# Performance work log

Measured on AMD Instinct MI355X. Metric: run time of the kernel, lower is better.

Reference implementation:

```python
import jax, jax.numpy as jnp
import numpy as np

CHUNK = 2048  # query points processed per step; bounds peak memory at [CHUNK, F, 3]


def _safe_div(num, den):
    den_s = jnp.where(jnp.abs(den) > 1e-12, den, 1.0)
    return num / den_s


def _closest_point_on_triangle(p, a, b, c):
    """Ericson's region-based closest point on triangle.
    p: [n,1,3], a/b/c: [1,F,3] -> returns [n,F,3]."""
    ab = b - a
    ac = c - a
    ap = p - a
    d1 = jnp.sum(ab * ap, -1)
    d2 = jnp.sum(ac * ap, -1)
    bp = p - b
    d3 = jnp.sum(ab * bp, -1)
    d4 = jnp.sum(ac * bp, -1)
    cpv = p - c
    d5 = jnp.sum(ab * cpv, -1)
    d6 = jnp.sum(ac * cpv, -1)
    vc = d1 * d4 - d3 * d2
    vb = d5 * d2 - d1 * d6
    va = d3 * d6 - d5 * d4
    v_ab = jnp.clip(_safe_div(d1, d1 - d3), 0.0, 1.0)
    w_ac = jnp.clip(_safe_div(d2, d2 - d6), 0.0, 1.0)
    w_bc = jnp.clip(_safe_div(d4 - d3, (d4 - d3) + (d5 - d6)), 0.0, 1.0)
    denom = va + vb + vc
    v = _safe_div(vb, denom)
    w = _safe_div(vc, denom)
    res = a + ab * v[..., None] + ac * w[..., None]  # face interior
    m_bc = (va <= 0) & ((d4 - d3) >= 0) & ((d5 - d6) >= 0)
    m_ac = (vb <= 0) & (d2 >= 0) & (d6 <= 0)
    m_ab = (vc <= 0) & (d1 >= 0) & (d3 <= 0)
    m_c = (d6 >= 0) & (d5 <= d6)
    m_b = (d3 >= 0) & (d4 <= d3)
    m_a = (d1 <= 0) & (d2 <= 0)
    res = jnp.where(m_bc[..., None], b + w_bc[..., None] * (c - b), res)
    res = jnp.where(m_ac[..., None], a + w_ac[..., None] * ac, res)
    res = jnp.where(m_ab[..., None], a + v_ab[..., None] * ab, res)
    res = jnp.where(m_c[..., None], c, res)
    res = jnp.where(m_b[..., None], b, res)
    res = jnp.where(m_a[..., None], a, res)
    return res


def _query_one_batch(tris, pts):
    # tris: [F,3,3], pts: [Q,3]
    a, b, c = tris[:, 0], tris[:, 1], tris[:, 2]

    def chunk_fn(pc):  # pc: [CHUNK,3]
        cp = _closest_point_on_triangle(pc[:, None, :], a[None], b[None], c[None])  # [CHUNK,F,3]
        d2 = jnp.sum((pc[:, None, :] - cp) ** 2, -1)  # [CHUNK,F] squared distances
        dist = jnp.min(d2, axis=-1)
        idx = jnp.argmin(d2, axis=-1)
        closest = jnp.take_along_axis(cp, idx[:, None, None], axis=1)[:, 0]
        return dist, closest, idx.astype(jnp.int32)

    Q = pts.shape[0]
    pts_c = pts.reshape(Q // CHUNK, CHUNK, 3)
    dist, closest, idx = jax.lax.map(chunk_fn, pts_c)
    return dist.reshape(Q), closest.reshape(Q, 3), idx.reshape(Q)


def setup_inputs() -> dict:
    key = jax.random.key(0)
    k1, k2 = jax.random.split(key)
    triangles = jax.random.normal(k1, (2, 4096, 3, 3), dtype=jnp.float32)
    points = jax.random.normal(k2, (2, 16384, 3), dtype=jnp.float32)
    return {"triangles": triangles, "points": points}


def reference(triangles, points):
    # distances are SQUARED point-to-mesh distances, matching the CUDA kernel
    distances, closest_points, closest_faces = jax.vmap(_query_one_batch)(triangles, points)
    return distances, closest_points, closest_faces
```

## Files before the change

### kernel.cpp

```cpp
#include <hip/hip_runtime.h>
#include <math.h>

namespace {

typedef float v2f __attribute__((ext_vector_type(2)));

constexpr int B = 2;
constexpr int F = 4096;
constexpr int Q = 16384;
constexpr int NP = B * Q;
constexpr int BLOCK = 256;
constexpr int P = 2;

constexpr int OFF_DIST = 0;
constexpr int OFF_CP = NP;
constexpr int OFF_FACE = 4 * NP;


__device__ __forceinline__ float safediv(float num, float den) {
  #pragma clang fp contract(off)
  float d = (fabsf(den) > 1e-12f) ? den : 1.0f;
  return num / d;
}

__device__ __forceinline__ float clamp01(float x) {
  return fminf(fmaxf(x, 0.0f), 1.0f);
}

__device__ __forceinline__ void closest_pt(
    float px, float py, float pz,
    float ax, float ay, float az,
    float bx, float by, float bz,
    float cx, float cy, float cz,
    float& rx, float& ry, float& rz) {
  #pragma clang fp contract(off)
  float abx = bx - ax, aby = by - ay, abz = bz - az;
  float acx = cx - ax, acy = cy - ay, acz = cz - az;
  float apx = px - ax, apy = py - ay, apz = pz - az;
  float d1 = (abx * apx + aby * apy) + abz * apz;
  float d2 = (acx * apx + acy * apy) + acz * apz;
  float bpx = px - bx, bpy = py - by, bpz = pz - bz;
  float d3 = (abx * bpx + aby * bpy) + abz * bpz;
  float d4 = (acx * bpx + acy * bpy) + acz * bpz;
  float cpx = px - cx, cpy = py - cy, cpz = pz - cz;
  float d5 = (abx * cpx + aby * cpy) + abz * cpz;
  float d6 = (acx * cpx + acy * cpy) + acz * cpz;

  float vc = d1 * d4 - d3 * d2;
  float vb = d5 * d2 - d1 * d6;
  float va = d3 * d6 - d5 * d4;

  float v_ab = clamp01(safediv(d1, d1 - d3));
  float w_ac = clamp01(safediv(d2, d2 - d6));
  float w_bc = clamp01(safediv(d4 - d3, (d4 - d3) + (d5 - d6)));

  float denom = (va + vb) + vc;
  float v = safediv(vb, denom);
  float w = safediv(vc, denom);

  float ox = ax + abx * v + acx * w;
  float oy = ay + aby * v + acy * w;
  float oz = az + abz * v + acz * w;

  bool m_bc = (va <= 0.0f) && (d4 - d3 >= 0.0f) && (d5 - d6 >= 0.0f);
  bool m_ac = (vb <= 0.0f) && (d2 >= 0.0f) && (d6 <= 0.0f);
  bool m_ab = (vc <= 0.0f) && (d1 >= 0.0f) && (d3 <= 0.0f);
  bool m_c  = (d6 >= 0.0f) && (d5 <= d6);
  bool m_b  = (d3 >= 0.0f) && (d4 <= d3);
  bool m_a  = (d1 <= 0.0f) && (d2 <= 0.0f);

  if (m_bc) { ox = bx + w_bc * (cx - bx); oy = by + w_bc * (cy - by); oz = bz + w_bc * (cz - bz); }
  if (m_ac) { ox = ax + w_ac * acx;       oy = ay + w_ac * acy;       oz = az + w_ac * acz; }
  if (m_ab) { ox = ax + v_ab * abx;       oy = ay + v_ab * aby;       oz = az + v_ab * abz; }
  if (m_c)  { ox = cx; oy = cy; oz = cz; }
  if (m_b)  { ox = bx; oy = by; oz = bz; }
  if (m_a)  { ox = ax; oy = ay; oz = az; }

  rx = ox; ry = oy; rz = oz;
}

__device__ __forceinline__ float exact_d2(
    float px, float py, float pz, const float* __restrict__ g ) {
  #pragma clang fp contract(off)
  float rx, ry, rz;
  closest_pt(px, py, pz,
             g[0], g[1], g[2], g[3], g[4], g[5], g[6], g[7], g[8],
             rx, ry, rz);
  float dx = px - rx, dy = py - ry, dz = pz - rz;
  return (dx * dx + dy * dy) + dz * dz;
}


__device__ __forceinline__ void ins4(unsigned key,
    unsigned& K1, unsigned& K2, unsigned& K3, unsigned& K4) {
  bool b1 = key < K1, b2 = key < K2, b3 = key < K3, b4 = key < K4;
  K4 = b3 ? K3 : (b4 ? key : K4);
  K3 = b2 ? K2 : (b3 ? key : K3);
  K2 = b1 ? K1 : (b2 ? key : K2);
  K1 = b1 ? key : K1;
}

__device__ __forceinline__ void ins8(unsigned key,
    unsigned& K1, unsigned& K2, unsigned& K3, unsigned& K4,
    unsigned& K5, unsigned& K6, unsigned& K7, unsigned& K8) {
  bool b1 = key < K1, b2 = key < K2, b3 = key < K3, b4 = key < K4;
  bool b5 = key < K5, b6 = key < K6, b7 = key < K7, b8 = key < K8;
  K8 = b7 ? K7 : (b8 ? key : K8);
  K7 = b6 ? K6 : (b7 ? key : K7);
  K6 = b5 ? K5 : (b6 ? key : K6);
  K5 = b4 ? K4 : (b5 ? key : K5);
  K4 = b3 ? K3 : (b4 ? key : K4);
  K3 = b2 ? K2 : (b3 ? key : K3);
  K2 = b1 ? K1 : (b2 ? key : K2);
  K1 = b1 ? key : K1;
}


__device__ __forceinline__ unsigned screen_fin(
    float dint, float tabm, float tacm, float tbcm,
    float td1, float td2, float ap2m, float bp2, float t43d,
    float va, float vb, float vc,
    float aa, float bb, float cc, float pp, int idx) {
  float tab = __builtin_amdgcn_fmed3f(tabm, 0.0f, 1.0f);
  float sab = fmaf(-tab, fmaf(-tab, aa, td1), ap2m);
  float tac = __builtin_amdgcn_fmed3f(tacm, 0.0f, 1.0f);
  float sac = fmaf(-tac, fmaf(-tac, bb, td2), ap2m);
  float tbc = __builtin_amdgcn_fmed3f(tbcm, 0.0f, 1.0f);
  float sbc = fmaf(-tbc, fmaf(-tbc, cc, t43d), bp2);
  float dseg = fminf(fminf(sab, sac), sbc);
  float mv   = fminf(fminf(va, vb), vc);
  float d = (mv > 0.0f) ? dint : dseg;
  d = fmaxf(d + pp, 0.0f);
  return (__float_as_uint(d) & 0xFFFFF000u) | (unsigned)idx;
}

template <int NC>
__global__ __launch_bounds__(BLOCK, 4) void bvh_screen(
    const float* __restrict__ tris,
    const float* __restrict__ pts,
    uint4* __restrict__ keys) {
  constexpr int CFL = F / NC;
  __shared__ float4 s_rec[5 * CFL];

  constexpr int BPB = (Q / P) / BLOCK;
  const int batch = blockIdx.x / BPB;
  const int j = (blockIdx.x % BPB) * BLOCK + threadIdx.x;
  const int chunk = blockIdx.y;
  const int tri0 = chunk * CFL;
  const float* tb = tris + (size_t)batch * F * 9;

  for (int t = threadIdx.x; t < CFL; t += BLOCK) {
    const float* g = tb + (size_t)(tri0 + t) * 9;
    float ax = g[0], ay = g[1], az = g[2];
    float abx = g[3] - ax, aby = g[4] - ay, abz = g[5] - az;
    float acx = g[6] - ax, acy = g[7] - ay, acz = g[8] - az;
    float aa   = abx * abx + aby * aby + abz * abz;
    float bb   = acx * acx + acy * acy + acz * acz;
    float abac = abx * acx + aby * acy + abz * acz;
    float bcx = acx - abx, bcy = acy - aby, bcz = acz - abz;
    float cc   = bcx * bcx + bcy * bcy + bcz * bcz;
    float nx = aby * acz - abz * acy;
    float ny = abz * acx - abx * acz;
    float nz = abx * acy - aby * acx;
    float n2 = nx * nx + ny * ny + nz * nz;
    float raa = (aa > 1e-12f) ? 1.0f / aa : 1.0f;
    float rbb = (bb > 1e-12f) ? 1.0f / bb : 1.0f;
    float rcc = (cc > 1e-12f) ? 1.0f / cc : 1.0f;
    float rdn = (n2 > 1e-12f) ? 1.0f / n2 : 1.0f;
    float c1 = -(ax * abx + ay * aby + az * abz);
    float c2 = -(ax * acx + ay * acy + az * acz);
    float caa2 = ax * ax + ay * ay + az * az;
    s_rec[0 * CFL + t] = make_float4(abx, aby, abz, c1);
    s_rec[1 * CFL + t] = make_float4(acx, acy, acz, c2);
    s_rec[2 * CFL + t] = make_float4(-2.0f * ax, -2.0f * ay, -2.0f * az, caa2);
    s_rec[3 * CFL + t] = make_float4(aa, bb, abac, cc);
    s_rec[4 * CFL + t] = make_float4(raa, rbb, rcc, rdn);
  }
  __syncthreads();

  const int p0 = batch * Q + j;
  const int p1 = p0 + Q / P;
  const float px0 = pts[p0 * 3 + 0], py0 = pts[p0 * 3 + 1], pz0 = pts[p0 * 3 + 2];
  const float px1 = pts[p1 * 3 + 0], py1 = pts[p1 * 3 + 1], pz1 = pts[p1 * 3 + 2];
  const v2f pxv = {px0, px1};
  const v2f pyv = {py0, py1};
  const v2f pzv = {pz0, pz1};
  const float pp0 = px0 * px0 + py0 * py0 + pz0 * pz0;
  const float pp1 = px1 * px1 + py1 * py1 + pz1 * pz1;

  unsigned A1 = ~0u, A2 = ~0u, A3 = ~0u, A4 = ~0u;
  unsigned Bk1 = ~0u, Bk2 = ~0u, Bk3 = ~0u, Bk4 = ~0u;

  {
    #pragma clang fp contract(fast)
    for (int t = 0; t < CFL; ++t) {
      const float4 R0 = s_rec[0 * CFL + t];
      const float4 R1 = s_rec[1 * CFL + t];
      const float4 R2 = s_rec[2 * CFL + t];
      const float4 R3 = s_rec[3 * CFL + t];
      const float4 R4 = s_rec[4 * CFL + t];

      v2f d1   = pxv * R0.x + pyv * R0.y + pzv * R0.z + R0.w;
      v2f d2   = pxv * R1.x + pyv * R1.y + pzv * R1.z + R1.w;
      v2f ap2m = pxv * R2.x + pyv * R2.y + pzv * R2.z + R2.w;
      v2f d3 = d1 - R3.x, d6 = d2 - R3.y, d4 = d2 - R3.z, d5 = d1 - R3.z;
      v2f t43 = d4 - d3;
      v2f va = d3 * d6 - d5 * d4;
      v2f vb = d5 * d2 - d1 * d6;
      v2f vc = d1 * d4 - d3 * d2;
      v2f td1 = d1 + d1, td2 = d2 + d2;
      v2f v = vb * R4.w, w = vc * R4.w;
      v2f h1 = v * R3.x + (w * R3.z - td1);
      v2f h2 = w * R3.y + (v * R3.z - td2);
      v2f dint = ap2m + (v * h1 + w * h2);
      v2f tabm = d1 * R4.x, tacm = d2 * R4.y, tbcm = t43 * R4.z;
      v2f bp2 = (ap2m - td1) + R3.x;
      v2f t43d = t43 + t43;

      unsigned kA = screen_fin(dint.x, tabm.x, tacm.x, tbcm.x,
                               td1.x, td2.x, ap2m.x, bp2.x, t43d.x,
                               va.x, vb.x, vc.x,
                               R3.x, R3.y, R3.w, pp0, tri0 + t);
      ins4(kA, A1, A2, A3, A4);
      unsigned kB = screen_fin(dint.y, tabm.y, tacm.y, tbcm.y,
                               td1.y, td2.y, ap2m.y, bp2.y, t43d.y,
                               va.y, vb.y, vc.y,
                               R3.x, R3.y, R3.w, pp1, tri0 + t);
      ins4(kB, Bk1, Bk2, Bk3, Bk4);
    }
  }

  keys[(size_t)chunk * NP + p0] = make_uint4(A1, A2, A3, A4);
  keys[(size_t)chunk * NP + p1] = make_uint4(Bk1, Bk2, Bk3, Bk4);
}

template <int NC>
__global__ __launch_bounds__(BLOCK) void bvh_finish(
    const float* __restrict__ tris,
    const float* __restrict__ pts,
    const uint4* __restrict__ keys,
    float* __restrict__ out) {
  const int gpt = blockIdx.x * BLOCK + threadIdx.x;
  if (gpt >= NP) return;

  unsigned K1 = ~0u, K2 = ~0u, K3 = ~0u, K4 = ~0u;
  unsigned K5 = ~0u, K6 = ~0u, K7 = ~0u, K8 = ~0u;
  for (int c = 0; c < NC; ++c) {
    uint4 k = keys[(size_t)c * NP + gpt];
    ins8(k.x, K1, K2, K3, K4, K5, K6, K7, K8);
    ins8(k.y, K1, K2, K3, K4, K5, K6, K7, K8);
    ins8(k.z, K1, K2, K3, K4, K5, K6, K7, K8);
    ins8(k.w, K1, K2, K3, K4, K5, K6, K7, K8);
  }

  const int batch = gpt / Q;
  const float* tb = tris + (size_t)batch * F * 9;
  const float px = pts[gpt * 3 + 0];
  const float py = pts[gpt * 3 + 1];
  const float pz = pts[gpt * 3 + 2];

  float be = INFINITY;
  int bi = 0x7FFFFFFF;
  #define CAND(Kx) { int t_ = (int)(Kx & 0xFFFu); \
    float d_ = exact_d2(px, py, pz, tb + (size_t)t_ * 9); \
    if (d_ < be || (d_ == be && t_ < bi)) { be = d_; bi = t_; } }
  CAND(K1) CAND(K2) CAND(K3) CAND(K4) CAND(K5) CAND(K6) CAND(K7) CAND(K8)
  #undef CAND

  const float* tr = tb + (size_t)bi * 9;
  float rx, ry, rz;
  closest_pt(px, py, pz,
             tr[0], tr[1], tr[2], tr[3], tr[4], tr[5], tr[6], tr[7], tr[8],
             rx, ry, rz);

  out[OFF_DIST + gpt] = be;
  out[OFF_CP + gpt * 3 + 0] = rx;
  out[OFF_CP + gpt * 3 + 1] = ry;
  out[OFF_CP + gpt * 3 + 2] = rz;
  out[OFF_FACE + gpt] = (float)bi;
}


__device__ __forceinline__ float screen_d2_sc(
    float px, float py, float pz,
    float ax, float ay, float az,
    float abx, float aby, float abz,
    float acx, float acy, float acz,
    float aa, float bb, float abac,
    float raa, float rbb, float rcc, float rdn) {
  #pragma clang fp contract(fast)
  float apx = px - ax, apy = py - ay, apz = pz - az;
  float ap2 = fmaf(apx, apx, fmaf(apy, apy, apz * apz));
  float d1  = fmaf(apx, abx, fmaf(apy, aby, apz * abz));
  float d2  = fmaf(apx, acx, fmaf(apy, acy, apz * acz));
  float d3 = d1 - aa, d6 = d2 - bb, d4 = d2 - abac, d5 = d1 - abac;
  float t43 = d4 - d3, t56 = d5 - d6;
  float va = d3 * d6 - d5 * d4;
  float vb = d5 * d2 - d1 * d6;
  float vc = d1 * d4 - d3 * d2;
  float td1 = d1 + d1, td2 = d2 + d2;
  float v = vb * rdn, w = vc * rdn;
  float h1 = fmaf(v, aa, fmaf(w, abac, -td1));
  float h2 = fmaf(w, bb, fmaf(v, abac, -td2));
  float dint = ap2 + fmaf(v, h1, w * h2);
  float tab = __builtin_amdgcn_fmed3f(d1 * raa, 0.0f, 1.0f);
  float sab = fmaf(-tab, fmaf(-tab, aa, td1), ap2);
  float tac = __builtin_amdgcn_fmed3f(d2 * rbb, 0.0f, 1.0f);
  float sac = fmaf(-tac, fmaf(-tac, bb, td2), ap2);
  float cc  = t43 + t56;
  float bp2 = (ap2 - td1) + aa;
  float tbc = __builtin_amdgcn_fmed3f(t43 * rcc, 0.0f, 1.0f);
  float sbc = fmaf(-tbc, fmaf(-tbc, cc, t43 + t43), bp2);
  float dseg = fminf(fminf(sab, sac), sbc);
  float mv   = fminf(fminf(va, vb), vc);
  float d = (mv > 0.0f) ? dint : dseg;
  return fmaxf(d, 0.0f);
}

__device__ __forceinline__ void tail4(
    const float* __restrict__ tb, int tri0,
    float px, float py, float pz,
    unsigned K1, unsigned K2, unsigned K3, unsigned K4,
    float& be, int& bi) {
  int c0 = (int)(K1 & 0x1FFu), c1 = (int)(K2 & 0x1FFu);
  int c2 = (int)(K3 & 0x1FFu), c3 = (int)(K4 & 0x1FFu);
  int tmp;
  if (c0 > c1) { tmp = c0; c0 = c1; c1 = tmp; }
  if (c2 > c3) { tmp = c2; c2 = c3; c3 = tmp; }
  if (c0 > c2) { tmp = c0; c0 = c2; c2 = tmp; }
  if (c1 > c3) { tmp = c1; c1 = c3; c3 = tmp; }
  if (c1 > c2) { tmp = c1; c1 = c2; c2 = tmp; }
  be = exact_d2(px, py, pz, tb + (size_t)(tri0 + c0) * 9);
  bi = c0;
  { float d = exact_d2(px, py, pz, tb + (size_t)(tri0 + c1) * 9);
    if (d < be) { be = d; bi = c1; } }
  { float d = exact_d2(px, py, pz, tb + (size_t)(tri0 + c2) * 9);
    if (d < be) { be = d; bi = c2; } }
  { float d = exact_d2(px, py, pz, tb + (size_t)(tri0 + c3) * 9);
    if (d < be) { be = d; bi = c3; } }
}

template <int NC>
__global__ __launch_bounds__(BLOCK, 4) void bvh_partial_p2(
    const float* __restrict__ tris,
    const float* __restrict__ pts,
    float* __restrict__ dbest,
    unsigned short* __restrict__ ibest) {
  constexpr int CFL = F / NC;
  __shared__ float4 s_rec[4 * CFL];

  constexpr int BPB = (Q / P) / BLOCK;
  const int batch = blockIdx.x / BPB;
  const int j = (blockIdx.x % BPB) * BLOCK + threadIdx.x;
  const int chunk = blockIdx.y;
  const int tri0 = chunk * CFL;
  const float* tb = tris + (size_t)batch * F * 9;

  for (int t = threadIdx.x; t < CFL; t += BLOCK) {
    const float* g = tb + (size_t)(tri0 + t) * 9;
    float ax = g[0], ay = g[1], az = g[2];
    float abx = g[3] - ax, aby = g[4] - ay, abz = g[5] - az;
    float acx = g[6] - ax, acy = g[7] - ay, acz = g[8] - az;
    float aa   = abx * abx + aby * aby + abz * abz;
    float bb   = acx * acx + acy * acy + acz * acz;
    float abac = abx * acx + aby * acy + abz * acz;
    float bcx = acx - abx, bcy = acy - aby, bcz = acz - abz;
    float cc   = bcx * bcx + bcy * bcy + bcz * bcz;
    float nx = aby * acz - abz * acy;
    float ny = abz * acx - abx * acz;
    float nz = abx * acy - aby * acx;
    float n2 = nx * nx + ny * ny + nz * nz;
    float raa = (aa > 1e-12f) ? 1.0f / aa : 1.0f;
    float rbb = (bb > 1e-12f) ? 1.0f / bb : 1.0f;
    float rcc = (cc > 1e-12f) ? 1.0f / cc : 1.0f;
    float rdn = (n2 > 1e-12f) ? 1.0f / n2 : 1.0f;
    s_rec[0 * CFL + t] = make_float4(ax, ay, az, abx);
    s_rec[1 * CFL + t] = make_float4(aby, abz, acx, acy);
    s_rec[2 * CFL + t] = make_float4(acz, aa, bb, abac);
    s_rec[3 * CFL + t] = make_float4(raa, rbb, rcc, rdn);
  }
  __syncthreads();

  const int p0 = batch * Q + j;
  const int p1 = p0 + Q / P;
  const float px0 = pts[p0 * 3 + 0], py0 = pts[p0 * 3 + 1], pz0 = pts[p0 * 3 + 2];
  const float px1 = pts[p1 * 3 + 0], py1 = pts[p1 * 3 + 1], pz1 = pts[p1 * 3 + 2];

  unsigned A1 = ~0u, A2 = ~0u, A3 = ~0u, A4 = ~0u;
  unsigned B1 = ~0u, B2 = ~0u, B3 = ~0u, B4 = ~0u;

  for (int t = 0; t < CFL; ++t) {
    const float4 R0 = s_rec[0 * CFL + t];
    const float4 R1 = s_rec[1 * CFL + t];
    const float4 R2 = s_rec[2 * CFL + t];
    const float4 R3 = s_rec[3 * CFL + t];
    float ax = R0.x, ay = R0.y, az = R0.z, abx = R0.w;
    float aby = R1.x, abz = R1.y, acx = R1.z, acy = R1.w;
    float acz = R2.x, aa = R2.y, bb = R2.z, abac = R2.w;
    float raa = R3.x, rbb = R3.y, rcc = R3.z, rdn = R3.w;

    float d0 = screen_d2_sc(px0, py0, pz0, ax, ay, az, abx, aby, abz,
                            acx, acy, acz, aa, bb, abac, raa, rbb, rcc, rdn);
    ins4((__float_as_uint(d0) & 0xFFFFFE00u) | (unsigned)t, A1, A2, A3, A4);
    float d1 = screen_d2_sc(px1, py1, pz1, ax, ay, az, abx, aby, abz,
                            acx, acy, acz, aa, bb, abac, raa, rbb, rcc, rdn);
    ins4((__float_as_uint(d1) & 0xFFFFFE00u) | (unsigned)t, B1, B2, B3, B4);
  }

  float be0, be1;
  int bi0, bi1;
  tail4(tb, tri0, px0, py0, pz0, A1, A2, A3, A4, be0, bi0);
  tail4(tb, tri0, px1, py1, pz1, B1, B2, B3, B4, be1, bi1);

  dbest[chunk * NP + p0] = be0;
  ibest[chunk * NP + p0] = (unsigned short)(tri0 + bi0);
  dbest[chunk * NP + p1] = be1;
  ibest[chunk * NP + p1] = (unsigned short)(tri0 + bi1);
}

template <int NC>
__global__ __launch_bounds__(BLOCK) void bvh_reduce(
    const float* __restrict__ tris,
    const float* __restrict__ pts,
    const float* __restrict__ dbest,
    const unsigned short* __restrict__ ibest,
    float* __restrict__ out) {
  const int gpt = blockIdx.x * BLOCK + threadIdx.x;
  if (gpt >= NP) return;

  float best = INFINITY;
  int bi = 0;
  for (int c = 0; c < NC; ++c) {
    float d = dbest[c * NP + gpt];
    if (d < best) { best = d; bi = ibest[c * NP + gpt]; }
  }

  const int batch = gpt / Q;
  const float px = pts[gpt * 3 + 0];
  const float py = pts[gpt * 3 + 1];
  const float pz = pts[gpt * 3 + 2];

  const float* tr = tris + ((size_t)batch * F + bi) * 9;
  float rx, ry, rz;
  closest_pt(px, py, pz,
             tr[0], tr[1], tr[2], tr[3], tr[4], tr[5], tr[6], tr[7], tr[8],
             rx, ry, rz);

  out[OFF_DIST + gpt] = best;
  out[OFF_CP + gpt * 3 + 0] = rx;
  out[OFF_CP + gpt * 3 + 1] = ry;
  out[OFF_CP + gpt * 3 + 2] = rz;
  out[OFF_FACE + gpt] = (float)bi;
}

}

extern "C" void kernel_launch(void* const* d_in, const int* in_sizes, int n_in,
                              void* d_out, int out_size, void* d_ws, size_t ws_size,
                              hipStream_t stream) {
  const float* tris = (const float*)d_in[0];
  const float* pts  = (const float*)d_in[1];
  float* out = (float*)d_out;

  const int gx = B * ((Q / P) / BLOCK);
  dim3 grid2((NP + BLOCK - 1) / BLOCK);

  constexpr size_t KEY16_BYTES = (size_t)16 * NP * sizeof(uint4);
  constexpr size_t NC16_BYTES  = (size_t)16 * NP * (sizeof(float) + sizeof(unsigned short));

  if (ws_size >= KEY16_BYTES) {
    uint4* keys = (uint4*)d_ws;
    bvh_screen<16><<<dim3(gx, 16), BLOCK, 0, stream>>>(tris, pts, keys);
    bvh_finish<16><<<grid2, BLOCK, 0, stream>>>(tris, pts, keys, out);
  } else if (ws_size >= NC16_BYTES) {
    float* dbest = (float*)d_ws;
    unsigned short* ibest = (unsigned short*)((char*)d_ws + (size_t)16 * NP * sizeof(float));
    bvh_partial_p2<16><<<dim3(gx, 16), BLOCK, 0, stream>>>(tris, pts, dbest, ibest);
    bvh_reduce<16><<<grid2, BLOCK, 0, stream>>>(tris, pts, dbest, ibest, out);
  } else {
    float* dbest = (float*)d_ws;
    unsigned short* ibest = (unsigned short*)((char*)d_ws + (size_t)8 * NP * sizeof(float));
    bvh_partial_p2<8><<<dim3(gx, 8), BLOCK, 0, stream>>>(tris, pts, dbest, ibest);
    bvh_reduce<8><<<grid2, BLOCK, 0, stream>>>(tris, pts, dbest, ibest, out);
  }
}
```

Before: 199.5 us.

## Screen four points per thread with 32 face chunks and top-2 keys

Result: faster. 166.8 us (-16.4%).

```diff
diff --git a/kernel.cpp b/kernel.cpp
--- a/kernel.cpp
+++ b/kernel.cpp
@@ -10,7 +10,7 @@
 constexpr int Q = 16384;
 constexpr int NP = B * Q;
 constexpr int BLOCK = 256;
-constexpr int P = 2;
+constexpr int P4 = 4;
 
 constexpr int OFF_DIST = 0;
 constexpr int OFF_CP = NP;
@@ -91,36 +91,35 @@
 }
 
 
-__device__ __forceinline__ void ins4(unsigned key,
-    unsigned& K1, unsigned& K2, unsigned& K3, unsigned& K4) {
-  bool b1 = key < K1, b2 = key < K2, b3 = key < K3, b4 = key < K4;
-  K4 = b3 ? K3 : (b4 ? key : K4);
-  K3 = b2 ? K2 : (b3 ? key : K3);
-  K2 = b1 ? K1 : (b2 ? key : K2);
-  K1 = b1 ? key : K1;
-}
-
-__device__ __forceinline__ void ins8(unsigned key,
+__device__ __forceinline__ unsigned umin2(unsigned a, unsigned b) { return a < b ? a : b; }
+__device__ __forceinline__ unsigned umax2(unsigned a, unsigned b) { return a > b ? a : b; }
+
+__device__ __forceinline__ void ins2(unsigned k, unsigned& K1, unsigned& K2) {
+  unsigned t = umax2(K1, k);
+  K1 = umin2(K1, k);
+  K2 = umin2(K2, t);
+}
+
+__device__ __forceinline__ void ins8(unsigned k,
     unsigned& K1, unsigned& K2, unsigned& K3, unsigned& K4,
     unsigned& K5, unsigned& K6, unsigned& K7, unsigned& K8) {
-  bool b1 = key < K1, b2 = key < K2, b3 = key < K3, b4 = key < K4;
-  bool b5 = key < K5, b6 = key < K6, b7 = key < K7, b8 = key < K8;
-  K8 = b7 ? K7 : (b8 ? key : K8);
-  K7 = b6 ? K6 : (b7 ? key : K7);
-  K6 = b5 ? K5 : (b6 ? key : K6);
-  K5 = b4 ? K4 : (b5 ? key : K5);
-  K4 = b3 ? K3 : (b4 ? key : K4);
-  K3 = b2 ? K2 : (b3 ? key : K3);
-  K2 = b1 ? K1 : (b2 ? key : K2);
-  K1 = b1 ? key : K1;
-}
-
-
-__device__ __forceinline__ unsigned screen_fin(
+  unsigned t;
+  t = umax2(K1, k); K1 = umin2(K1, k);
+  k = t; t = umax2(K2, k); K2 = umin2(K2, k);
+  k = t; t = umax2(K3, k); K3 = umin2(K3, k);
+  k = t; t = umax2(K4, k); K4 = umin2(K4, k);
+  k = t; t = umax2(K5, k); K5 = umin2(K5, k);
+  k = t; t = umax2(K6, k); K6 = umin2(K6, k);
+  k = t; t = umax2(K7, k); K7 = umin2(K7, k);
+  K8 = umin2(K8, t);
+}
+
+
+__device__ __forceinline__ unsigned fin_one(
     float dint, float tabm, float tacm, float tbcm,
     float td1, float td2, float ap2m, float bp2, float t43d,
     float va, float vb, float vc,
-    float aa, float bb, float cc, float pp, int idx) {
+    float aa, float bb, float cc, float pp, int gidx) {
   float tab = __builtin_amdgcn_fmed3f(tabm, 0.0f, 1.0f);
   float sab = fmaf(-tab, fmaf(-tab, aa, td1), ap2m);
   float tac = __builtin_amdgcn_fmed3f(tacm, 0.0f, 1.0f);
@@ -131,18 +130,18 @@
   float mv   = fminf(fminf(va, vb), vc);
   float d = (mv > 0.0f) ? dint : dseg;
   d = fmaxf(d + pp, 0.0f);
-  return (__float_as_uint(d) & 0xFFFFF000u) | (unsigned)idx;
+  return (__float_as_uint(d) & 0xFFFFF000u) | (unsigned)gidx;
 }
 
 template <int NC>
-__global__ __launch_bounds__(BLOCK, 4) void bvh_screen(
+__global__ __launch_bounds__(BLOCK, 4) void bvh_screen4(
     const float* __restrict__ tris,
     const float* __restrict__ pts,
-    uint4* __restrict__ keys) {
+    uint2* __restrict__ keys) {
   constexpr int CFL = F / NC;
   __shared__ float4 s_rec[5 * CFL];
 
-  constexpr int BPB = (Q / P) / BLOCK;
+  constexpr int BPB = (Q / P4) / BLOCK;
   const int batch = blockIdx.x / BPB;
   const int j = (blockIdx.x % BPB) * BLOCK + threadIdx.x;
   const int chunk = blockIdx.y;
@@ -179,17 +178,20 @@
   __syncthreads();
 
   const int p0 = batch * Q + j;
-  const int p1 = p0 + Q / P;
-  const float px0 = pts[p0 * 3 + 0], py0 = pts[p0 * 3 + 1], pz0 = pts[p0 * 3 + 2];
-  const float px1 = pts[p1 * 3 + 0], py1 = pts[p1 * 3 + 1], pz1 = pts[p1 * 3 + 2];
-  const v2f pxv = {px0, px1};
-  const v2f pyv = {py0, py1};
-  const v2f pzv = {pz0, pz1};
-  const float pp0 = px0 * px0 + py0 * py0 + pz0 * pz0;
-  const float pp1 = px1 * px1 + py1 * py1 + pz1 * pz1;
-
-  unsigned A1 = ~0u, A2 = ~0u, A3 = ~0u, A4 = ~0u;
-  unsigned Bk1 = ~0u, Bk2 = ~0u, Bk3 = ~0u, Bk4 = ~0u;
+  float px0 = pts[(p0          ) * 3 + 0], py0 = pts[(p0          ) * 3 + 1], pz0 = pts[(p0          ) * 3 + 2];
+  float px1 = pts[(p0 + Q/4    ) * 3 + 0], py1 = pts[(p0 + Q/4    ) * 3 + 1], pz1 = pts[(p0 + Q/4    ) * 3 + 2];
+  float px2 = pts[(p0 + Q/2    ) * 3 + 0], py2 = pts[(p0 + Q/2    ) * 3 + 1], pz2 = pts[(p0 + Q/2    ) * 3 + 2];
+  float px3 = pts[(p0 + 3*(Q/4)) * 3 + 0], py3 = pts[(p0 + 3*(Q/4)) * 3 + 1], pz3 = pts[(p0 + 3*(Q/4)) * 3 + 2];
+
+  const v2f pxA = {px0, px1}, pyA = {py0, py1}, pzA = {pz0, pz1};
+  const v2f pxB = {px2, px3}, pyB = {py2, py3}, pzB = {pz2, pz3};
+  const float pp0 = px0*px0 + py0*py0 + pz0*pz0;
+  const float pp1 = px1*px1 + py1*py1 + pz1*pz1;
+  const float pp2 = px2*px2 + py2*py2 + pz2*pz2;
+  const float pp3 = px3*px3 + py3*py3 + pz3*pz3;
+
+  unsigned A1 = ~0u, A2 = ~0u, Bk1 = ~0u, Bk2 = ~0u;
+  unsigned C1 = ~0u, C2 = ~0u, D1 = ~0u, D2 = ~0u;
 
   {
     #pragma clang fp contract(fast)
@@ -199,46 +201,71 @@
       const float4 R2 = s_rec[2 * CFL + t];
       const float4 R3 = s_rec[3 * CFL + t];
       const float4 R4 = s_rec[4 * CFL + t];
-
-      v2f d1   = pxv * R0.x + pyv * R0.y + pzv * R0.z + R0.w;
-      v2f d2   = pxv * R1.x + pyv * R1.y + pzv * R1.z + R1.w;
-      v2f ap2m = pxv * R2.x + pyv * R2.y + pzv * R2.z + R2.w;
-      v2f d3 = d1 - R3.x, d6 = d2 - R3.y, d4 = d2 - R3.z, d5 = d1 - R3.z;
-      v2f t43 = d4 - d3;
-      v2f va = d3 * d6 - d5 * d4;
-      v2f vb = d5 * d2 - d1 * d6;
-      v2f vc = d1 * d4 - d3 * d2;
-      v2f td1 = d1 + d1, td2 = d2 + d2;
-      v2f v = vb * R4.w, w = vc * R4.w;
-      v2f h1 = v * R3.x + (w * R3.z - td1);
-      v2f h2 = w * R3.y + (v * R3.z - td2);
-      v2f dint = ap2m + (v * h1 + w * h2);
-      v2f tabm = d1 * R4.x, tacm = d2 * R4.y, tbcm = t43 * R4.z;
-      v2f bp2 = (ap2m - td1) + R3.x;
-      v2f t43d = t43 + t43;
-
-      unsigned kA = screen_fin(dint.x, tabm.x, tacm.x, tbcm.x,
-                               td1.x, td2.x, ap2m.x, bp2.x, t43d.x,
-                               va.x, vb.x, vc.x,
-                               R3.x, R3.y, R3.w, pp0, tri0 + t);
-      ins4(kA, A1, A2, A3, A4);
-      unsigned kB = screen_fin(dint.y, tabm.y, tacm.y, tbcm.y,
-                               td1.y, td2.y, ap2m.y, bp2.y, t43d.y,
-                               va.y, vb.y, vc.y,
-                               R3.x, R3.y, R3.w, pp1, tri0 + t);
-      ins4(kB, Bk1, Bk2, Bk3, Bk4);
+      const int gidx = tri0 + t;
+
+      {
+        v2f d1   = pxA * R0.x + pyA * R0.y + pzA * R0.z + R0.w;
+        v2f d2   = pxA * R1.x + pyA * R1.y + pzA * R1.z + R1.w;
+        v2f ap2m = pxA * R2.x + pyA * R2.y + pzA * R2.z + R2.w;
+        v2f d3 = d1 - R3.x, d6 = d2 - R3.y, d4 = d2 - R3.z, d5 = d1 - R3.z;
+        v2f t43 = d4 - d3;
+        v2f va = d3 * d6 - d5 * d4;
+        v2f vb = d5 * d2 - d1 * d6;
+        v2f vc = d1 * d4 - d3 * d2;
+        v2f td1 = d1 + d1, td2 = d2 + d2;
+        v2f v = vb * R4.w, w = vc * R4.w;
+        v2f h1 = v * R3.x + (w * R3.z - td1);
+        v2f h2 = w * R3.y + (v * R3.z - td2);
+        v2f dint = ap2m + (v * h1 + w * h2);
+        v2f tabm = d1 * R4.x, tacm = d2 * R4.y, tbcm = t43 * R4.z;
+        v2f bp2 = (ap2m - td1) + R3.x;
+        v2f t43d = t43 + t43;
+        ins2(fin_one(dint.x, tabm.x, tacm.x, tbcm.x, td1.x, td2.x, ap2m.x,
+                     bp2.x, t43d.x, va.x, vb.x, vc.x,
+                     R3.x, R3.y, R3.w, pp0, gidx), A1, A2);
+        ins2(fin_one(dint.y, tabm.y, tacm.y, tbcm.y, td1.y, td2.y, ap2m.y,
+                     bp2.y, t43d.y, va.y, vb.y, vc.y,
+                     R3.x, R3.y, R3.w, pp1, gidx), Bk1, Bk2);
+      }
+      {
+        v2f d1   = pxB * R0.x + pyB * R0.y + pzB * R0.z + R0.w;
+        v2f d2   = pxB * R1.x + pyB * R1.y + pzB * R1.z + R1.w;
+        v2f ap2m = pxB * R2.x + pyB * R2.y + pzB * R2.z + R2.w;
+        v2f d3 = d1 - R3.x, d6 = d2 - R3.y, d4 = d2 - R3.z, d5 = d1 - R3.z;
+        v2f t43 = d4 - d3;
+        v2f va = d3 * d6 - d5 * d4;
+        v2f vb = d5 * d2 - d1 * d6;
+        v2f vc = d1 * d4 - d3 * d2;
+        v2f td1 = d1 + d1, td2 = d2 + d2;
+        v2f v = vb * R4.w, w = vc * R4.w;
+        v2f h1 = v * R3.x + (w * R3.z - td1);
+        v2f h2 = w * R3.y + (v * R3.z - td2);
+        v2f dint = ap2m + (v * h1 + w * h2);
+        v2f tabm = d1 * R4.x, tacm = d2 * R4.y, tbcm = t43 * R4.z;
+        v2f bp2 = (ap2m - td1) + R3.x;
+        v2f t43d = t43 + t43;
+        ins2(fin_one(dint.x, tabm.x, tacm.x, tbcm.x, td1.x, td2.x, ap2m.x,
+                     bp2.x, t43d.x, va.x, vb.x, vc.x,
+                     R3.x, R3.y, R3.w, pp2, gidx), C1, C2);
+        ins2(fin_one(dint.y, tabm.y, tacm.y, tbcm.y, td1.y, td2.y, ap2m.y,
+                     bp2.y, t43d.y, va.y, vb.y, vc.y,
+                     R3.x, R3.y, R3.w, pp3, gidx), D1, D2);
+      }
     }
   }
 
-  keys[(size_t)chunk * NP + p0] = make_uint4(A1, A2, A3, A4);
-  keys[(size_t)chunk * NP + p1] = make_uint4(Bk1, Bk2, Bk3, Bk4);
-}
+  keys[(size_t)chunk * NP + p0            ] = make_uint2(A1, A2);
+  keys[(size_t)chunk * NP + p0 + Q/4      ] = make_uint2(Bk1, Bk2);
+  keys[(size_t)chunk * NP + p0 + Q/2      ] = make_uint2(C1, C2);
+  keys[(size_t)chunk * NP + p0 + 3*(Q/4)  ] = make_uint2(D1, D2);
+}
+
 
 template <int NC>
-__global__ __launch_bounds__(BLOCK) void bvh_finish(
+__global__ __launch_bounds__(BLOCK) void bvh_finish2(
     const float* __restrict__ tris,
     const float* __restrict__ pts,
-    const uint4* __restrict__ keys,
+    const uint2* __restrict__ keys,
     float* __restrict__ out) {
   const int gpt = blockIdx.x * BLOCK + threadIdx.x;
   if (gpt >= NP) return;
@@ -246,11 +273,9 @@
   unsigned K1 = ~0u, K2 = ~0u, K3 = ~0u, K4 = ~0u;
   unsigned K5 = ~0u, K6 = ~0u, K7 = ~0u, K8 = ~0u;
   for (int c = 0; c < NC; ++c) {
-    uint4 k = keys[(size_t)c * NP + gpt];
+    uint2 k = keys[(size_t)c * NP + gpt];
     ins8(k.x, K1, K2, K3, K4, K5, K6, K7, K8);
     ins8(k.y, K1, K2, K3, K4, K5, K6, K7, K8);
-    ins8(k.z, K1, K2, K3, K4, K5, K6, K7, K8);
-    ins8(k.w, K1, K2, K3, K4, K5, K6, K7, K8);
   }
 
   const int batch = gpt / Q;
@@ -317,6 +342,15 @@
   return fmaxf(d, 0.0f);
 }
 
+__device__ __forceinline__ void ins4c(unsigned key,
+    unsigned& K1, unsigned& K2, unsigned& K3, unsigned& K4) {
+  bool b1 = key < K1, b2 = key < K2, b3 = key < K3, b4 = key < K4;
+  K4 = b3 ? K3 : (b4 ? key : K4);
+  K3 = b2 ? K2 : (b3 ? key : K3);
+  K2 = b1 ? K1 : (b2 ? key : K2);
+  K1 = b1 ? key : K1;
+}
+
 __device__ __forceinline__ void tail4(
     const float* __restrict__ tb, int tri0,
     float px, float py, float pz,
@@ -349,7 +383,7 @@
   constexpr int CFL = F / NC;
   __shared__ float4 s_rec[4 * CFL];
 
-  constexpr int BPB = (Q / P) / BLOCK;
+  constexpr int BPB = (Q / 2) / BLOCK;
   const int batch = blockIdx.x / BPB;
   const int j = (blockIdx.x % BPB) * BLOCK + threadIdx.x;
   const int chunk = blockIdx.y;
@@ -382,7 +416,7 @@
   __syncthreads();
 
   const int p0 = batch * Q + j;
-  const int p1 = p0 + Q / P;
+  const int p1 = p0 + Q / 2;
   const float px0 = pts[p0 * 3 + 0], py0 = pts[p0 * 3 + 1], pz0 = pts[p0 * 3 + 2];
   const float px1 = pts[p1 * 3 + 0], py1 = pts[p1 * 3 + 1], pz1 = pts[p1 * 3 + 2];
 
@@ -401,10 +435,10 @@
 
     float d0 = screen_d2_sc(px0, py0, pz0, ax, ay, az, abx, aby, abz,
                             acx, acy, acz, aa, bb, abac, raa, rbb, rcc, rdn);
-    ins4((__float_as_uint(d0) & 0xFFFFFE00u) | (unsigned)t, A1, A2, A3, A4);
+    ins4c((__float_as_uint(d0) & 0xFFFFFE00u) | (unsigned)t, A1, A2, A3, A4);
     float d1 = screen_d2_sc(px1, py1, pz1, ax, ay, az, abx, aby, abz,
                             acx, acy, acz, aa, bb, abac, raa, rbb, rcc, rdn);
-    ins4((__float_as_uint(d1) & 0xFFFFFE00u) | (unsigned)t, B1, B2, B3, B4);
+    ins4c((__float_as_uint(d1) & 0xFFFFFE00u) | (unsigned)t, B1, B2, B3, B4);
   }
 
   float be0, be1;
@@ -462,24 +496,20 @@
   const float* pts  = (const float*)d_in[1];
   float* out = (float*)d_out;
 
-  const int gx = B * ((Q / P) / BLOCK);
   dim3 grid2((NP + BLOCK - 1) / BLOCK);
 
-  constexpr size_t KEY16_BYTES = (size_t)16 * NP * sizeof(uint4);
-  constexpr size_t NC16_BYTES  = (size_t)16 * NP * (sizeof(float) + sizeof(unsigned short));
-
-  if (ws_size >= KEY16_BYTES) {
-    uint4* keys = (uint4*)d_ws;
-    bvh_screen<16><<<dim3(gx, 16), BLOCK, 0, stream>>>(tris, pts, keys);
-    bvh_finish<16><<<grid2, BLOCK, 0, stream>>>(tris, pts, keys, out);
-  } else if (ws_size >= NC16_BYTES) {
-    float* dbest = (float*)d_ws;
-    unsigned short* ibest = (unsigned short*)((char*)d_ws + (size_t)16 * NP * sizeof(float));
-    bvh_partial_p2<16><<<dim3(gx, 16), BLOCK, 0, stream>>>(tris, pts, dbest, ibest);
-    bvh_reduce<16><<<grid2, BLOCK, 0, stream>>>(tris, pts, dbest, ibest, out);
+  constexpr int NC = 32;
+  constexpr size_t KEY_BYTES = (size_t)NC * NP * sizeof(uint2);
+
+  if (ws_size >= KEY_BYTES) {
+    uint2* keys = (uint2*)d_ws;
+    const int gx = B * ((Q / P4) / BLOCK);
+    bvh_screen4<NC><<<dim3(gx, NC), BLOCK, 0, stream>>>(tris, pts, keys);
+    bvh_finish2<NC><<<grid2, BLOCK, 0, stream>>>(tris, pts, keys, out);
   } else {
     float* dbest = (float*)d_ws;
     unsigned short* ibest = (unsigned short*)((char*)d_ws + (size_t)8 * NP * sizeof(float));
+    const int gx = B * ((Q / 2) / BLOCK);
     bvh_partial_p2<8><<<dim3(gx, 8), BLOCK, 0, stream>>>(tris, pts, dbest, ibest);
     bvh_reduce<8><<<grid2, BLOCK, 0, stream>>>(tris, pts, dbest, ibest, out);
   }
```
